# Performance work log

Measured on AMD Instinct MI355X. Metric: run time of the kernel, lower is better.

## Reference

```python
import jax, jax.numpy as jnp
import numpy as np

H = 16
D_MODEL = 1024
D_K = D_MODEL // H


def setup_inputs() -> dict:
    key = jax.random.key(0)
    ks = jax.random.split(key, 12)
    B, S = 4, 2048
    scale = 1.0 / np.sqrt(D_MODEL)
    inp = {
        "query": jax.random.normal(ks[0], (B, S, D_MODEL), dtype=jnp.float32),
        "key": jax.random.normal(ks[1], (B, S, D_MODEL), dtype=jnp.float32),
        "value": jax.random.normal(ks[2], (B, S, D_MODEL), dtype=jnp.float32),
        "Wq": jax.random.normal(ks[3], (D_MODEL, D_MODEL), dtype=jnp.float32) * scale,
        "bq": jnp.zeros((D_MODEL,), dtype=jnp.float32),
        "Wk": jax.random.normal(ks[4], (D_MODEL, D_MODEL), dtype=jnp.float32) * scale,
        "bk": jnp.zeros((D_MODEL,), dtype=jnp.float32),
        "Wv": jax.random.normal(ks[5], (D_MODEL, D_MODEL), dtype=jnp.float32) * scale,
        "bv": jnp.zeros((D_MODEL,), dtype=jnp.float32),
        "Wo": jax.random.normal(ks[6], (D_MODEL, D_MODEL), dtype=jnp.float32) * scale,
        "bo": jnp.zeros((D_MODEL,), dtype=jnp.float32),
    }
    return inp


def reference(query, key, value, Wq, bq, Wk, bk, Wv, bv, Wo, bo):
    B, S, _ = query.shape
    # Linear projections (torch Linear: x @ W^T + b), then split heads -> [B,H,S,d_k]
    def proj(x, W, b):
        y = x @ W.T + b
        return y.reshape(B, S, H, D_K).transpose(0, 2, 1, 3)

    q = proj(query, Wq, bq)
    k = proj(key, Wk, bk)
    v = proj(value, Wv, bv)

    # Explicit QK^T / sqrt(d_k), softmax, AV (no mask; dropout = identity in eval)
    scores = jnp.einsum("bhqd,bhkd->bhqk", q, k) / jnp.sqrt(jnp.float32(D_K))
    attn = jax.nn.softmax(scores, axis=-1)
    x = jnp.einsum("bhqk,bhkd->bhqd", attn, v)

    # Merge heads and final output projection
    x = x.transpose(0, 2, 1, 3).reshape(B, S, H * D_K)
    return x @ Wo.T + bo
```

## Files before the change

kernel.cpp:

```cpp
#include <hip/hip_runtime.h>
#include <hip/hip_bf16.h>
#include <stdint.h>

#define BATCH 4
#define SEQ   2048
#define DM    1024
#define NH    16
#define DK    64
#define MROWS (BATCH * SEQ)

#define C1 0.1803368801111204f

typedef __attribute__((ext_vector_type(8))) short short8;
typedef __attribute__((ext_vector_type(4))) float f32x4;
typedef __attribute__((ext_vector_type(4))) float floatv4;
typedef __attribute__((ext_vector_type(4))) unsigned short us4;
typedef __attribute__((ext_vector_type(4))) unsigned int uint4v;

static __device__ __forceinline__ unsigned short f2bf(float f) {
    union { float f; uint32_t u; } c; c.f = f;
    uint32_t u = c.u;
    return (unsigned short)((u + 0x7fffu + ((u >> 16) & 1u)) >> 16);
}

static __device__ __forceinline__ unsigned int cvt_pk_bf16(float a, float b) {
    __hip_bfloat162 h = __float22bfloat162_rn(float2{a, b});
    unsigned int u; __builtin_memcpy(&u, &h, 4); return u;
}

static __device__ __forceinline__ float ex2(float x) { return __builtin_amdgcn_exp2f(x); }

#define AS1C(p) ((const __attribute__((address_space(1))) unsigned int*)(uintptr_t)(const void*)(p))
#define AS3(p)  ((__attribute__((address_space(3))) unsigned int*)(uintptr_t)(void*)(p))

__global__ __launch_bounds__(256) void cvt3_k(const float* __restrict__ a, const float* __restrict__ b,
                                              const float* __restrict__ c,
                                              unsigned short* __restrict__ oa, unsigned short* __restrict__ ob,
                                              unsigned short* __restrict__ oc) {
    const int z = blockIdx.y;
    const float* s = (z == 0) ? a : (z == 1) ? b : c;
    unsigned short* o = (z == 0) ? oa : (z == 1) ? ob : oc;
    int i = blockIdx.x * 256 + threadIdx.x;
    floatv4 v = ((const floatv4*)s)[i];
    us4 w; w.x = f2bf(v.x); w.y = f2bf(v.y); w.z = f2bf(v.z); w.w = f2bf(v.w);
    ((us4*)o)[i] = w;
}

__global__ __launch_bounds__(256) void cvt4_k(const float* __restrict__ a, const float* __restrict__ b,
                                              const float* __restrict__ c, const float* __restrict__ d,
                                              unsigned short* __restrict__ oa, unsigned short* __restrict__ ob,
                                              unsigned short* __restrict__ oc, unsigned short* __restrict__ od) {
    const int z = blockIdx.y;
    const float* s = (z == 0) ? a : (z == 1) ? b : (z == 2) ? c : d;
    unsigned short* o = (z == 0) ? oa : (z == 1) ? ob : (z == 2) ? oc : od;
    int i = blockIdx.x * 256 + threadIdx.x;
    floatv4 v = ((const floatv4*)s)[i];
    us4 w; w.x = f2bf(v.x); w.y = f2bf(v.y); w.z = f2bf(v.z); w.w = f2bf(v.w);
    ((us4*)o)[i] = w;
}

template <int MODE>
static __device__ __forceinline__ void gemm256_body(const unsigned short* __restrict__ A,
                                                    const unsigned short* __restrict__ Bw,
                                                    const float* __restrict__ bias,
                                                    void* __restrict__ out, int m0, int n0,
                                                    float scale) {
    constexpr int K = DM;
    constexpr int NK = K / 64;
    constexpr int NIT = NK / 2;

    const int tid = threadIdx.x;
    const int wave = tid >> 6, lane = tid & 63, quad = lane >> 4, l16 = lane & 15;
    const int wm = wave >> 2, wn = wave & 3;

    __shared__ alignas(16) unsigned short AsU[4 * 8192];
    __shared__ alignas(16) unsigned short BsU[4 * 8192];

    f32x4 acc[8][4];
    #pragma unroll
    for (int i = 0; i < 8; i++)
        #pragma unroll
        for (int j = 0; j < 4; j++) acc[i][j] = (f32x4){0.f, 0.f, 0.f, 0.f};

    const int sl   = (lane & 7) ^ (lane >> 3);
    const int grow = wave * 16 + (lane >> 3) * 2 + (sl >> 2);
    const int gc8  = (sl & 3) * 8;
    const unsigned short* Ag = A  + (size_t)(m0 + grow) * K + gc8;
    const unsigned short* Bg = Bw + (size_t)(n0 + grow) * K + gc8;

    const int sx8 = ((((l16 & 1) * 4 + quad) ^ (l16 >> 1)) * 8);
    const int la  = wm * 4096 + (l16 >> 1) * 64 + sx8;
    const int lb  = wn * 2048 + (l16 >> 1) * 64 + sx8;

    short8 af[8], bfr[4];

#define G256_STG(GP, LDSP, b, kh, kt)                                                     \
    {   _Pragma("unroll")                                                                 \
        for (int s_ = 0; s_ < 2; s_++)                                                    \
            __builtin_amdgcn_global_load_lds(                                             \
                AS1C(GP + (size_t)s_ * 128 * K + (kt) * 64 + (kh) * 32),                  \
                AS3(LDSP + ((b) * 2 + (kh)) * 8192 + s_ * 4096 + wave * 512), 16, 0, 0); }

#define G256_LD(b, kh)                                                                    \
    {   const int rg_ = ((b) * 2 + (kh)) * 8192;                                          \
        _Pragma("unroll")                                                                 \
        for (int mf_ = 0; mf_ < 8; mf_++) af[mf_] = *(const short8*)&AsU[rg_ + la + mf_ * 512]; \
        _Pragma("unroll")                                                                 \
        for (int nf_ = 0; nf_ < 4; nf_++) bfr[nf_] = *(const short8*)&BsU[rg_ + lb + nf_ * 512]; }

#define G256_MMA(nh)                                                                      \
    {   __builtin_amdgcn_s_setprio(1);                                                    \
        _Pragma("unroll")                                                                 \
        for (int mf_ = 0; mf_ < 8; mf_++) {                                               \
            acc[mf_][2*(nh)]   = __builtin_amdgcn_mfma_f32_16x16x32_bf16(af[mf_], bfr[2*(nh)],   acc[mf_][2*(nh)],   0, 0, 0); \
            acc[mf_][2*(nh)+1] = __builtin_amdgcn_mfma_f32_16x16x32_bf16(af[mf_], bfr[2*(nh)+1], acc[mf_][2*(nh)+1], 0, 0, 0); } \
        __builtin_amdgcn_s_setprio(0); }

#define G256_VM10 asm volatile("s_waitcnt vmcnt(10)" ::: "memory")
#define G256_VM0  asm volatile("s_waitcnt vmcnt(0)"  ::: "memory")
#define G256_LG0  { asm volatile("s_waitcnt lgkmcnt(0)" ::: "memory"); __builtin_amdgcn_sched_barrier(0); }
#define G256_BAR  __builtin_amdgcn_s_barrier()
#define G256_SB0  __builtin_amdgcn_sched_barrier(0)

    G256_STG(Ag, AsU, 0, 0, 0); G256_STG(Bg, BsU, 0, 0, 0);
    G256_STG(Ag, AsU, 0, 1, 0); G256_STG(Bg, BsU, 0, 1, 0);
    G256_STG(Ag, AsU, 1, 0, 1); G256_STG(Bg, BsU, 1, 0, 1);
    G256_STG(Ag, AsU, 1, 1, 1);

    #pragma unroll 1
    for (int i = 0; i < NIT - 1; ++i) {
        const int t2 = 2 * i + 2, t3 = 2 * i + 3;
        G256_VM10; G256_BAR; G256_SB0;
        G256_STG(Bg, BsU, 1, 1, 2 * i + 1);
        G256_LD(0, 0); G256_LG0; G256_MMA(0); G256_BAR;
        G256_STG(Ag, AsU, 0, 0, t2); G256_MMA(1);
        G256_VM10; G256_BAR; G256_SB0;
        G256_STG(Bg, BsU, 0, 0, t2);
        G256_LD(0, 1); G256_LG0; G256_MMA(0); G256_BAR;
        G256_STG(Ag, AsU, 0, 1, t2); G256_MMA(1);
        G256_VM10; G256_BAR; G256_SB0;
        G256_STG(Bg, BsU, 0, 1, t2);
        G256_LD(1, 0); G256_LG0; G256_MMA(0); G256_BAR;
        G256_STG(Ag, AsU, 1, 0, t3); G256_MMA(1);
        G256_VM10; G256_BAR; G256_SB0;
        G256_STG(Bg, BsU, 1, 0, t3);
        G256_LD(1, 1); G256_LG0; G256_MMA(0); G256_BAR;
        G256_STG(Ag, AsU, 1, 1, t3); G256_MMA(1);
    }
    G256_STG(Bg, BsU, 1, 1, NK - 1);
    G256_VM0; G256_BAR; G256_SB0;
    G256_LD(0, 0); G256_LG0; G256_MMA(0); G256_MMA(1);
    G256_LD(0, 1); G256_LG0; G256_MMA(0); G256_MMA(1);
    G256_LD(1, 0); G256_LG0; G256_MMA(0); G256_MMA(1);
    G256_LD(1, 1); G256_LG0; G256_MMA(0); G256_MMA(1);

#undef G256_STG
#undef G256_LD
#undef G256_MMA
#undef G256_VM10
#undef G256_VM0
#undef G256_LG0
#undef G256_BAR
#undef G256_SB0

    #pragma unroll
    for (int nf = 0; nf < 4; nf++) {
        const int n = n0 + wn * 64 + nf * 16 + l16;
        const float bv = bias[n];
        if (MODE == 2) {
            const int bb = m0 >> 11;
            const int hh = n >> 6, dd = n & (DK - 1);
            unsigned short* obase = (unsigned short*)out
                                  + (((size_t)bb * NH + hh) * DK + dd) * SEQ
                                  + (m0 & (SEQ - 1)) + wm * 128 + quad * 8;
            #pragma unroll
            for (int mf = 0; mf < 8; mf++) {
                us4 w;
                #pragma unroll
                for (int r = 0; r < 4; r++) w[r] = f2bf(acc[mf][nf][r] + bv);
                *(us4*)(obase + (mf >> 1) * 32 + (mf & 1) * 4) = w;
            }
        } else {
            const int hh = n >> 6, dd = n & (DK - 1);
            #pragma unroll
            for (int mf = 0; mf < 8; mf++) {
                #pragma unroll
                for (int r = 0; r < 4; r++) {
                    const int mrow = m0 + wm * 128 + mf * 16 + quad * 4 + r;
                    float val = (acc[mf][nf][r] + bv) * scale;
                    if (MODE == 0) {
                        int bb = mrow >> 11, ss = mrow & (SEQ - 1);
                        ((unsigned short*)out)[((((size_t)bb * NH + hh) * SEQ + ss) << 6) + dd] = f2bf(val);
                    } else {
                        ((float*)out)[(size_t)mrow * DM + n] = val;
                    }
                }
            }
        }
    }
}

__global__ __launch_bounds__(512, 1) void gemm_qk_k(const unsigned short* qa, const unsigned short* ka,
                                                    const unsigned short* wq, const unsigned short* wk,
                                                    const float* bq, const float* bk,
                                                    unsigned short* qh, unsigned short* kh) {
    const int z = blockIdx.z;
    const unsigned short* A = (z == 0) ? qa : ka;
    const unsigned short* W = (z == 0) ? wq : wk;
    const float* bi = (z == 0) ? bq : bk;
    unsigned short* o = (z == 0) ? qh : kh;
    const float sc = (z == 0) ? C1 : 1.0f;
    gemm256_body<0>(A, W, bi, o, blockIdx.x * 256, blockIdx.y * 256, sc);
}

__global__ __launch_bounds__(512, 1) void gemm_v_k(const unsigned short* va, const unsigned short* wv,
                                                   const float* bv, unsigned short* vtc) {
    gemm256_body<2>(va, wv, bv, vtc, blockIdx.x * 256, blockIdx.y * 256, 1.0f);
}

__global__ __launch_bounds__(512, 1) void gemm_o_k(const unsigned short* xb, const unsigned short* wo,
                                                   const float* bo, float* out) {
    gemm256_body<1>(xb, wo, bo, out, blockIdx.x * 256, blockIdx.y * 256, 1.0f);
}

__global__ __launch_bounds__(256, 4) void flash_attn_k(const unsigned short* __restrict__ Qh,
                                                       const unsigned short* __restrict__ Kh,
                                                       const unsigned short* __restrict__ Vtc,
                                                       unsigned short* __restrict__ Xb) {
    const int tid = threadIdx.x;
    const int wave = tid >> 6, lane = tid & 63, quad = lane >> 4, l16 = lane & 15;
    const int h = blockIdx.y, b = blockIdx.z;
    const unsigned short* Qp = Qh  + (size_t)(b * NH + h) * SEQ * DK;
    const unsigned short* Kp = Kh  + (size_t)(b * NH + h) * SEQ * DK;
    const unsigned short* Vp = Vtc + (size_t)(b * NH + h) * DK * SEQ;
    const int q0 = blockIdx.x * 128 + wave * 32;

    __shared__ alignas(16) unsigned short kt[128][72];
    __shared__ alignas(16) unsigned short vt[64][136];

    short8 aq[2][2];
    #pragma unroll
    for (int m = 0; m < 2; m++)
        #pragma unroll
        for (int kk = 0; kk < 2; kk++)
            aq[m][kk] = *(const short8*)(Qp + (size_t)(q0 + m * 16 + l16) * DK + kk * 32 + quad * 8);

    short8 ones;
    #pragma unroll
    for (int j = 0; j < 8; j++) ones[j] = (short)0x3F80;

    f32x4 O[2][4];
    f32x4 lacc[2];
    #pragma unroll
    for (int m = 0; m < 2; m++) {
        #pragma unroll
        for (int db = 0; db < 4; db++) O[m][db] = (f32x4){0.f, 0.f, 0.f, 0.f};
        lacc[m] = (f32x4){0.f, 0.f, 0.f, 0.f};
    }

    const unsigned short* kgp = Kp + (size_t)(tid >> 3) * DK + (tid & 7) * 8;
    const unsigned short* vgp = Vp + (size_t)(tid >> 4) * SEQ + (tid & 15) * 8;
    unsigned short* kws = &kt[tid >> 3][(tid & 7) * 8];
    unsigned short* vws = &vt[tid >> 4][(tid & 15) * 8];

    short8 krg[4], vrg[4];
    #pragma unroll
    for (int it = 0; it < 4; it++) {
        krg[it] = *(const short8*)(kgp + (size_t)it * 32 * DK);
        vrg[it] = *(const short8*)(vgp + (size_t)it * 16 * SEQ);
    }
    kgp += (size_t)128 * DK;
    vgp += 128;

    for (int t0 = 0; t0 < SEQ; t0 += 128) {
        __syncthreads();
        #pragma unroll
        for (int it = 0; it < 4; it++) {
            *(short8*)(kws + it * 32 * 72) = krg[it];
            *(short8*)(vws + it * 16 * 136) = vrg[it];
        }
        #pragma unroll
        for (int it = 0; it < 4; it++) {
            krg[it] = *(const short8*)(kgp + (size_t)it * 32 * DK);
            vrg[it] = *(const short8*)(vgp + (size_t)it * 16 * SEQ);
        }
        kgp += (size_t)128 * DK;
        vgp += 128;
        asm volatile("s_waitcnt lgkmcnt(0)" ::: "memory");
        __builtin_amdgcn_s_barrier();
        __builtin_amdgcn_sched_barrier(0);

        #pragma unroll
        for (int t = 0; t < 4; t++) {
            f32x4 s[2][2];
            #pragma unroll
            for (int m = 0; m < 2; m++)
                #pragma unroll
                for (int sb = 0; sb < 2; sb++) s[m][sb] = (f32x4){0.f, 0.f, 0.f, 0.f};

            #pragma unroll
            for (int kk = 0; kk < 2; kk++) {
                short8 bk0 = *(const short8*)&kt[(t * 2    ) * 16 + l16][kk * 32 + quad * 8];
                short8 bk1 = *(const short8*)&kt[(t * 2 + 1) * 16 + l16][kk * 32 + quad * 8];
                s[0][0] = __builtin_amdgcn_mfma_f32_16x16x32_bf16(bk0, aq[0][kk], s[0][0], 0, 0, 0);
                s[0][1] = __builtin_amdgcn_mfma_f32_16x16x32_bf16(bk1, aq[0][kk], s[0][1], 0, 0, 0);
                s[1][0] = __builtin_amdgcn_mfma_f32_16x16x32_bf16(bk0, aq[1][kk], s[1][0], 0, 0, 0);
                s[1][1] = __builtin_amdgcn_mfma_f32_16x16x32_bf16(bk1, aq[1][kk], s[1][1], 0, 0, 0);
            }

            short8 pa[2];
            #pragma unroll
            for (int m = 0; m < 2; m++) {
                uint4v pk;
                pk.x = cvt_pk_bf16(ex2(s[m][0][0]), ex2(s[m][0][1]));
                pk.y = cvt_pk_bf16(ex2(s[m][0][2]), ex2(s[m][0][3]));
                pk.z = cvt_pk_bf16(ex2(s[m][1][0]), ex2(s[m][1][1]));
                pk.w = cvt_pk_bf16(ex2(s[m][1][2]), ex2(s[m][1][3]));
                __builtin_memcpy(&pa[m], &pk, 16);
            }

            #pragma unroll
            for (int db = 0; db < 4; db++) {
                short8 vf = *(const short8*)&vt[db * 16 + l16][t * 32 + quad * 8];
                O[0][db] = __builtin_amdgcn_mfma_f32_16x16x32_bf16(pa[0], vf, O[0][db], 0, 0, 0);
                O[1][db] = __builtin_amdgcn_mfma_f32_16x16x32_bf16(pa[1], vf, O[1][db], 0, 0, 0);
            }
            lacc[0] = __builtin_amdgcn_mfma_f32_16x16x32_bf16(pa[0], ones, lacc[0], 0, 0, 0);
            lacc[1] = __builtin_amdgcn_mfma_f32_16x16x32_bf16(pa[1], ones, lacc[1], 0, 0, 0);
        }
    }

    #pragma unroll
    for (int m = 0; m < 2; m++) {
        #pragma unroll
        for (int r = 0; r < 4; r++) {
            const float inv = 1.f / lacc[m][r];
            const int srow = q0 + m * 16 + quad * 4 + r;
            unsigned short* op = Xb + ((size_t)b * SEQ + srow) * DM + h * DK;
            #pragma unroll
            for (int db = 0; db < 4; db++)
                op[db * 16 + l16] = f2bf(O[m][db][r] * inv);
        }
    }
}

extern "C" void kernel_launch(void* const* d_in, const int* in_sizes, int n_in,
                              void* d_out, int out_size, void* d_ws, size_t ws_size,
                              hipStream_t stream) {
    const float* q_in = (const float*)d_in[0];
    const float* k_in = (const float*)d_in[1];
    const float* v_in = (const float*)d_in[2];
    const float* Wq   = (const float*)d_in[3];
    const float* bq   = (const float*)d_in[4];
    const float* Wk   = (const float*)d_in[5];
    const float* bk   = (const float*)d_in[6];
    const float* Wv   = (const float*)d_in[7];
    const float* bv   = (const float*)d_in[8];
    const float* Wo   = (const float*)d_in[9];
    const float* bo   = (const float*)d_in[10];

    const size_t MB = 1024ull * 1024ull;
    char* ws = (char*)d_ws;
    unsigned short* qa  = (unsigned short*)(ws +   0 * MB);
    unsigned short* ka  = (unsigned short*)(ws +  16 * MB);
    unsigned short* va  = (unsigned short*)(ws +  32 * MB);
    unsigned short* wqb = (unsigned short*)(ws +  48 * MB);
    unsigned short* wkb = (unsigned short*)(ws +  50 * MB);
    unsigned short* wvb = (unsigned short*)(ws +  52 * MB);
    unsigned short* wob = (unsigned short*)(ws +  54 * MB);
    unsigned short* qh  = (unsigned short*)(ws +  56 * MB);
    unsigned short* kh  = (unsigned short*)(ws +  72 * MB);
    unsigned short* vtc = (unsigned short*)(ws +  88 * MB);
    unsigned short* xb  = (unsigned short*)(ws + 104 * MB);

    cvt3_k<<<dim3(8192, 3), 256, 0, stream>>>(q_in, k_in, v_in, qa, ka, va);
    cvt4_k<<<dim3(1024, 4), 256, 0, stream>>>(Wq, Wk, Wv, Wo, wqb, wkb, wvb, wob);

    gemm_qk_k<<<dim3(MROWS / 256, DM / 256, 2), 512, 0, stream>>>(qa, ka, wqb, wkb,
                                                                  bq, bk, qh, kh);
    gemm_v_k<<<dim3(MROWS / 256, DM / 256), 512, 0, stream>>>(va, wvb, bv, vtc);

    flash_attn_k<<<dim3(SEQ / 128, NH, BATCH), 256, 0, stream>>>(qh, kh, vtc, xb);

    gemm_o_k<<<dim3(MROWS / 256, DM / 256), 512, 0, stream>>>(xb, wob, bo, (float*)d_out);
}
```

Measured before the change: 349.4 us.

## Merge QKV projection launches and double per-wave query rows in attention

The Q/K and V projection GEMMs are folded into one launch with a z-dimension of 3, and the epilogue mode becomes a runtime argument instead of a template parameter. The flash attention kernel now processes 64 query rows per wave (256 per block) instead of 32, so each K/V tile loaded into shared memory feeds twice as many MFMAs. Launch bounds drop to 2 blocks per CU to allow the extra registers. The costs are higher register pressure, half as many attention blocks, and a runtime branch in the GEMM epilogue.

```diff
diff --git a/kernel.cpp b/kernel.cpp
--- a/kernel.cpp
+++ b/kernel.cpp
@@ -59,12 +59,11 @@
     ((us4*)o)[i] = w;
 }
 
-template <int MODE>
 static __device__ __forceinline__ void gemm256_body(const unsigned short* __restrict__ A,
                                                     const unsigned short* __restrict__ Bw,
                                                     const float* __restrict__ bias,
                                                     void* __restrict__ out, int m0, int n0,
-                                                    float scale) {
+                                                    float scale, int mode) {
     constexpr int K = DM;
     constexpr int NK = K / 64;
     constexpr int NIT = NK / 2;
@@ -167,7 +166,7 @@
     for (int nf = 0; nf < 4; nf++) {
         const int n = n0 + wn * 64 + nf * 16 + l16;
         const float bv = bias[n];
-        if (MODE == 2) {
+        if (mode == 2) {
             const int bb = m0 >> 11;
             const int hh = n >> 6, dd = n & (DK - 1);
             unsigned short* obase = (unsigned short*)out
@@ -188,7 +187,7 @@
                 for (int r = 0; r < 4; r++) {
                     const int mrow = m0 + wm * 128 + mf * 16 + quad * 4 + r;
                     float val = (acc[mf][nf][r] + bv) * scale;
-                    if (MODE == 0) {
+                    if (mode == 0) {
                         int bb = mrow >> 11, ss = mrow & (SEQ - 1);
                         ((unsigned short*)out)[((((size_t)bb * NH + hh) * SEQ + ss) << 6) + dd] = f2bf(val);
                     } else {
@@ -200,30 +199,28 @@
     }
 }
 
-__global__ __launch_bounds__(512, 1) void gemm_qk_k(const unsigned short* qa, const unsigned short* ka,
-                                                    const unsigned short* wq, const unsigned short* wk,
-                                                    const float* bq, const float* bk,
-                                                    unsigned short* qh, unsigned short* kh) {
+__global__ __launch_bounds__(512, 1) void gemm_qkv_k(const unsigned short* qa, const unsigned short* ka,
+                                                     const unsigned short* va, const unsigned short* wq,
+                                                     const unsigned short* wk, const unsigned short* wv,
+                                                     const float* bq, const float* bk, const float* bv,
+                                                     unsigned short* qh, unsigned short* kh,
+                                                     unsigned short* vtc) {
     const int z = blockIdx.z;
-    const unsigned short* A = (z == 0) ? qa : ka;
-    const unsigned short* W = (z == 0) ? wq : wk;
-    const float* bi = (z == 0) ? bq : bk;
-    unsigned short* o = (z == 0) ? qh : kh;
+    const unsigned short* A = (z == 0) ? qa : (z == 1) ? ka : va;
+    const unsigned short* W = (z == 0) ? wq : (z == 1) ? wk : wv;
+    const float* bi = (z == 0) ? bq : (z == 1) ? bk : bv;
+    void* o = (z == 0) ? (void*)qh : (z == 1) ? (void*)kh : (void*)vtc;
     const float sc = (z == 0) ? C1 : 1.0f;
-    gemm256_body<0>(A, W, bi, o, blockIdx.x * 256, blockIdx.y * 256, sc);
-}
-
-__global__ __launch_bounds__(512, 1) void gemm_v_k(const unsigned short* va, const unsigned short* wv,
-                                                   const float* bv, unsigned short* vtc) {
-    gemm256_body<2>(va, wv, bv, vtc, blockIdx.x * 256, blockIdx.y * 256, 1.0f);
+    const int mode = (z == 2) ? 2 : 0;
+    gemm256_body(A, W, bi, o, blockIdx.x * 256, blockIdx.y * 256, sc, mode);
 }
 
 __global__ __launch_bounds__(512, 1) void gemm_o_k(const unsigned short* xb, const unsigned short* wo,
                                                    const float* bo, float* out) {
-    gemm256_body<1>(xb, wo, bo, out, blockIdx.x * 256, blockIdx.y * 256, 1.0f);
-}
-
-__global__ __launch_bounds__(256, 4) void flash_attn_k(const unsigned short* __restrict__ Qh,
+    gemm256_body(xb, wo, bo, out, blockIdx.x * 256, blockIdx.y * 256, 1.0f, 1);
+}
+
+__global__ __launch_bounds__(256, 2) void flash_attn_k(const unsigned short* __restrict__ Qh,
                                                        const unsigned short* __restrict__ Kh,
                                                        const unsigned short* __restrict__ Vtc,
                                                        unsigned short* __restrict__ Xb) {
@@ -233,14 +230,14 @@
     const unsigned short* Qp = Qh  + (size_t)(b * NH + h) * SEQ * DK;
     const unsigned short* Kp = Kh  + (size_t)(b * NH + h) * SEQ * DK;
     const unsigned short* Vp = Vtc + (size_t)(b * NH + h) * DK * SEQ;
-    const int q0 = blockIdx.x * 128 + wave * 32;
+    const int q0 = blockIdx.x * 256 + wave * 64;
 
     __shared__ alignas(16) unsigned short kt[128][72];
     __shared__ alignas(16) unsigned short vt[64][136];
 
-    short8 aq[2][2];
-    #pragma unroll
-    for (int m = 0; m < 2; m++)
+    short8 aq[4][2];
+    #pragma unroll
+    for (int m = 0; m < 4; m++)
         #pragma unroll
         for (int kk = 0; kk < 2; kk++)
             aq[m][kk] = *(const short8*)(Qp + (size_t)(q0 + m * 16 + l16) * DK + kk * 32 + quad * 8);
@@ -249,10 +246,10 @@
     #pragma unroll
     for (int j = 0; j < 8; j++) ones[j] = (short)0x3F80;
 
-    f32x4 O[2][4];
-    f32x4 lacc[2];
-    #pragma unroll
-    for (int m = 0; m < 2; m++) {
+    f32x4 O[4][4];
+    f32x4 lacc[4];
+    #pragma unroll
+    for (int m = 0; m < 4; m++) {
         #pragma unroll
         for (int db = 0; db < 4; db++) O[m][db] = (f32x4){0.f, 0.f, 0.f, 0.f};
         lacc[m] = (f32x4){0.f, 0.f, 0.f, 0.f};
@@ -292,9 +289,9 @@
 
         #pragma unroll
         for (int t = 0; t < 4; t++) {
-            f32x4 s[2][2];
-            #pragma unroll
-            for (int m = 0; m < 2; m++)
+            f32x4 s[4][2];
+            #pragma unroll
+            for (int m = 0; m < 4; m++)
                 #pragma unroll
                 for (int sb = 0; sb < 2; sb++) s[m][sb] = (f32x4){0.f, 0.f, 0.f, 0.f};
 
@@ -302,15 +299,16 @@
             for (int kk = 0; kk < 2; kk++) {
                 short8 bk0 = *(const short8*)&kt[(t * 2    ) * 16 + l16][kk * 32 + quad * 8];
                 short8 bk1 = *(const short8*)&kt[(t * 2 + 1) * 16 + l16][kk * 32 + quad * 8];
-                s[0][0] = __builtin_amdgcn_mfma_f32_16x16x32_bf16(bk0, aq[0][kk], s[0][0], 0, 0, 0);
-                s[0][1] = __builtin_amdgcn_mfma_f32_16x16x32_bf16(bk1, aq[0][kk], s[0][1], 0, 0, 0);
-                s[1][0] = __builtin_amdgcn_mfma_f32_16x16x32_bf16(bk0, aq[1][kk], s[1][0], 0, 0, 0);
-                s[1][1] = __builtin_amdgcn_mfma_f32_16x16x32_bf16(bk1, aq[1][kk], s[1][1], 0, 0, 0);
-            }
-
-            short8 pa[2];
-            #pragma unroll
-            for (int m = 0; m < 2; m++) {
+                #pragma unroll
+                for (int m = 0; m < 4; m++) {
+                    s[m][0] = __builtin_amdgcn_mfma_f32_16x16x32_bf16(bk0, aq[m][kk], s[m][0], 0, 0, 0);
+                    s[m][1] = __builtin_amdgcn_mfma_f32_16x16x32_bf16(bk1, aq[m][kk], s[m][1], 0, 0, 0);
+                }
+            }
+
+            short8 pa[4];
+            #pragma unroll
+            for (int m = 0; m < 4; m++) {
                 uint4v pk;
                 pk.x = cvt_pk_bf16(ex2(s[m][0][0]), ex2(s[m][0][1]));
                 pk.y = cvt_pk_bf16(ex2(s[m][0][2]), ex2(s[m][0][3]));
@@ -322,16 +320,18 @@
             #pragma unroll
             for (int db = 0; db < 4; db++) {
                 short8 vf = *(const short8*)&vt[db * 16 + l16][t * 32 + quad * 8];
-                O[0][db] = __builtin_amdgcn_mfma_f32_16x16x32_bf16(pa[0], vf, O[0][db], 0, 0, 0);
-                O[1][db] = __builtin_amdgcn_mfma_f32_16x16x32_bf16(pa[1], vf, O[1][db], 0, 0, 0);
-            }
-            lacc[0] = __builtin_amdgcn_mfma_f32_16x16x32_bf16(pa[0], ones, lacc[0], 0, 0, 0);
-            lacc[1] = __builtin_amdgcn_mfma_f32_16x16x32_bf16(pa[1], ones, lacc[1], 0, 0, 0);
-        }
-    }
-
-    #pragma unroll
-    for (int m = 0; m < 2; m++) {
+                #pragma unroll
+                for (int m = 0; m < 4; m++)
+                    O[m][db] = __builtin_amdgcn_mfma_f32_16x16x32_bf16(pa[m], vf, O[m][db], 0, 0, 0);
+            }
+            #pragma unroll
+            for (int m = 0; m < 4; m++)
+                lacc[m] = __builtin_amdgcn_mfma_f32_16x16x32_bf16(pa[m], ones, lacc[m], 0, 0, 0);
+        }
+    }
+
+    #pragma unroll
+    for (int m = 0; m < 4; m++) {
         #pragma unroll
         for (int r = 0; r < 4; r++) {
             const float inv = 1.f / lacc[m][r];
@@ -376,11 +376,10 @@
     cvt3_k<<<dim3(8192, 3), 256, 0, stream>>>(q_in, k_in, v_in, qa, ka, va);
     cvt4_k<<<dim3(1024, 4), 256, 0, stream>>>(Wq, Wk, Wv, Wo, wqb, wkb, wvb, wob);
 
-    gemm_qk_k<<<dim3(MROWS / 256, DM / 256, 2), 512, 0, stream>>>(qa, ka, wqb, wkb,
-                                                                  bq, bk, qh, kh);
-    gemm_v_k<<<dim3(MROWS / 256, DM / 256), 512, 0, stream>>>(va, wvb, bv, vtc);
-
-    flash_attn_k<<<dim3(SEQ / 128, NH, BATCH), 256, 0, stream>>>(qh, kh, vtc, xb);
+    gemm_qkv_k<<<dim3(MROWS / 256, DM / 256, 3), 512, 0, stream>>>(qa, ka, va, wqb, wkb, wvb,
+                                                                   bq, bk, bv, qh, kh, vtc);
+
+    flash_attn_k<<<dim3(SEQ / 256, NH, BATCH), 256, 0, stream>>>(qh, kh, vtc, xb);
 
     gemm_o_k<<<dim3(MROWS / 256, DM / 256), 512, 0, stream>>>(xb, wob, bo, (float*)d_out);
 }
```

Result: faster. 341.0 us (-2.4%).
